# Performance work log

Measured on AMD Instinct MI355X. Metric: run time of the kernel, lower is better.

Reference implementation:

```python
import jax, jax.numpy as jnp
import numpy as np

B = 1 << 20
EMB = 8
N_BREEDS, N_TEMPS = 15, 9
HIDDENS = [128, 64, 32]
IN_DIM = (EMB * 2 + 9) * 2  # 50
EPS = 1e-5


def _encode_pet(breed, size, energy, temp, age, social, weight, breed_emb, temp_emb):
    # breed/temp: [B] int -> embedding gather [B,8]; size/energy -> one-hot [B,3]
    be = breed_emb[breed]
    te = temp_emb[temp]
    size_oh = jax.nn.one_hot(size, 3, dtype=be.dtype)
    energy_oh = jax.nn.one_hot(energy, 3, dtype=be.dtype)
    nums = jnp.stack([age / 15.0, social, weight / 100.0], axis=-1)  # [B,3]
    return jnp.concatenate([be, size_oh, energy_oh, te, nums], axis=-1)  # [B,25]


def _mlp(x, Ws, bs, gammas, betas, Wout, bout):
    for W, b, g, bt in zip(Ws, bs, gammas, betas):
        x = x @ W + b
        mu = jnp.mean(x, axis=0)
        var = jnp.mean(jnp.square(x - mu), axis=0)  # biased var (torch BN training)
        x = (x - mu) * jax.lax.rsqrt(var + EPS) * g + bt
        x = jax.nn.relu(x)
    x = x @ Wout + bout
    return jax.nn.sigmoid(x).squeeze(-1)  # [B]


def setup_inputs() -> dict:
    key = jax.random.key(0)
    ks = jax.random.split(key, 32)
    inp = {
        "pet1_breed": jax.random.randint(ks[0], (B,), 0, N_BREEDS, dtype=jnp.int32),
        "pet1_size": jax.random.randint(ks[1], (B,), 0, 3, dtype=jnp.int32),
        "pet1_energy": jax.random.randint(ks[2], (B,), 0, 3, dtype=jnp.int32),
        "pet1_temp": jax.random.randint(ks[3], (B,), 0, N_TEMPS, dtype=jnp.int32),
        "pet1_age": jax.random.uniform(ks[4], (B,)) * 15.0,
        "pet1_social": jax.random.uniform(ks[5], (B,)),
        "pet1_weight": jax.random.uniform(ks[6], (B,)) * 100.0,
        "pet2_breed": jax.random.randint(ks[7], (B,), 0, N_BREEDS, dtype=jnp.int32),
        "pet2_size": jax.random.randint(ks[8], (B,), 0, 3, dtype=jnp.int32),
        "pet2_energy": jax.random.randint(ks[9], (B,), 0, 3, dtype=jnp.int32),
        "pet2_temp": jax.random.randint(ks[10], (B,), 0, N_TEMPS, dtype=jnp.int32),
        "pet2_age": jax.random.uniform(ks[11], (B,)) * 15.0,
        "pet2_social": jax.random.uniform(ks[12], (B,)),
        "pet2_weight": jax.random.uniform(ks[13], (B,)) * 100.0,
        "breed_emb": jax.random.normal(ks[14], (N_BREEDS, EMB), dtype=jnp.float32),
        "temp_emb": jax.random.normal(ks[15], (N_TEMPS, EMB), dtype=jnp.float32),
    }
    prev = IN_DIM
    ki = 16
    for i, h in enumerate(HIDDENS, start=1):
        s = 1.0 / np.sqrt(prev)
        inp[f"W{i}"] = jax.random.uniform(ks[ki], (prev, h), minval=-s, maxval=s); ki += 1
        inp[f"b{i}"] = jax.random.uniform(ks[ki], (h,), minval=-s, maxval=s); ki += 1
        inp[f"gamma{i}"] = jnp.ones((h,), jnp.float32)
        inp[f"beta{i}"] = jnp.zeros((h,), jnp.float32)
        prev = h
    s = 1.0 / np.sqrt(prev)
    inp["W4"] = jax.random.uniform(ks[ki], (prev, 1), minval=-s, maxval=s); ki += 1
    inp["b4"] = jax.random.uniform(ks[ki], (1,), minval=-s, maxval=s)
    return inp


def reference(pet1_breed, pet1_size, pet1_energy, pet1_temp, pet1_age, pet1_social, pet1_weight,
              pet2_breed, pet2_size, pet2_energy, pet2_temp, pet2_age, pet2_social, pet2_weight,
              breed_emb, temp_emb,
              W1, b1, gamma1, beta1, W2, b2, gamma2, beta2, W3, b3, gamma3, beta3, W4, b4):
    f1 = _encode_pet(pet1_breed, pet1_size, pet1_energy, pet1_temp,
                     pet1_age, pet1_social, pet1_weight, breed_emb, temp_emb)
    f2 = _encode_pet(pet2_breed, pet2_size, pet2_energy, pet2_temp,
                     pet2_age, pet2_social, pet2_weight, breed_emb, temp_emb)
    x = jnp.concatenate([f1, f2], axis=-1)  # [B,50]
    return _mlp(x, [W1, W2, W3], [b1, b2, b3], [gamma1, gamma2, gamma3],
                [beta1, beta2, beta3], W4, b4)
```

## Files before the change

kernel.cpp:

```cpp
#include <hip/hip_runtime.h>
#include <hip/hip_bf16.h>

#define BATCH (1u<<20)
static constexpr float EPSBN = 1e-5f;
static constexpr float INV_B = 1.0f / (float)BATCH;

typedef unsigned int   uint;
typedef unsigned short ushort;

#define TSTR 132
#define NTABROWS 66
#define OFF_W2F    55296ULL
#define OFF_W3F    71680ULL
#define OFF_STATS  75776ULL
#define OFF_PARAMS 90112ULL
#define OFF_X2     98304ULL
#define OFF_X3D    (98304ULL + 134217728ULL)
#define T1_NEED    (98304ULL + 134217728ULL)
#define T2_NEED    (98304ULL + 134217728ULL + 67108864ULL)

struct Ptrs {
  const int *br1,*sz1,*en1,*tp1; const float *ag1,*so1,*wt1;
  const int *br2,*sz2,*en2,*tp2; const float *ag2,*so2,*wt2;
  const float *bemb,*temb;
  const float *W1,*b1,*g1,*be1;
  const float *W2,*b2,*g2,*be2;
  const float *W3,*b3,*g3,*be3;
  const float *W4,*b4;
  float* ws; float* out;
};

typedef __attribute__((ext_vector_type(8))) short bf16x8;
typedef __attribute__((ext_vector_type(4))) float f32x4;

__device__ __forceinline__ float4 ld4(const float* p) {
  return *reinterpret_cast<const float4*>(p);
}
__device__ __forceinline__ float4 f4add(float4 a, float4 b) {
  return make_float4(a.x+b.x, a.y+b.y, a.z+b.z, a.w+b.w);
}
__device__ __forceinline__ float4 f4fma(float4 a, float4 w, float s) {
  return make_float4(fmaf(w.x,s,a.x), fmaf(w.y,s,a.y), fmaf(w.z,s,a.z), fmaf(w.w,s,a.w));
}
__device__ __forceinline__ void add4(float4& a, const float4 b) {
  a.x += b.x; a.y += b.y; a.z += b.z; a.w += b.w;
}
__device__ __forceinline__ void fma4s(float4& a, const float4 b, float s) {
  a.x = fmaf(b.x, s, a.x); a.y = fmaf(b.y, s, a.y);
  a.z = fmaf(b.z, s, a.z); a.w = fmaf(b.w, s, a.w);
}

__device__ __forceinline__ ushort bfb(float f) {
  union { __hip_bfloat16 h; ushort u; } cv; cv.h = __float2bfloat16(f); return cv.u;
}
__device__ __forceinline__ uint pk2(float a, float b) {
  return ((uint)bfb(b) << 16) | (uint)bfb(a);
}
__device__ __forceinline__ bf16x8 ldfrag(const void* p) {
  union { uint4 u; bf16x8 v; } cv; cv.u = *reinterpret_cast<const uint4*>(p); return cv.v;
}
__device__ __forceinline__ bf16x8 mkfrag(uint a, uint b, uint c, uint d) {
  union { uint4 u; bf16x8 v; } cv; cv.u = make_uint4(a,b,c,d); return cv.v;
}
__device__ __forceinline__ float bflo(uint w) { return __uint_as_float(w << 16); }
__device__ __forceinline__ float bfhi(uint w) { return __uint_as_float(w & 0xffff0000u); }

struct SIdx { int r[8]; float v[6]; };
__device__ __forceinline__ SIdx load_idx(const Ptrs& P, unsigned s) {
  SIdx o;
  o.r[0] = P.br1[s];      o.r[1] = 15 + P.tp1[s];
  o.r[2] = 24 + P.br2[s]; o.r[3] = 39 + P.tp2[s];
  o.r[4] = 48 + P.sz1[s]; o.r[5] = 51 + P.en1[s];
  o.r[6] = 54 + P.sz2[s]; o.r[7] = 57 + P.en2[s];
  o.v[0] = P.ag1[s]*(1.0f/15.0f); o.v[1] = P.so1[s]; o.v[2] = P.wt1[s]*0.01f;
  o.v[3] = P.ag2[s]*(1.0f/15.0f); o.v[4] = P.so2[s]; o.v[5] = P.wt2[s]*0.01f;
  return o;
}

__device__ __forceinline__ float4 gather4(const float* Tl, const float* contT,
                                          const int rb[8], const float v[6], int c) {
  float4 A = f4add(f4add(ld4(Tl+rb[0]+c), ld4(Tl+rb[1]+c)),
                   f4add(ld4(Tl+rb[2]+c), ld4(Tl+rb[3]+c)));
  float4 B = f4add(f4add(ld4(Tl+rb[4]+c), ld4(Tl+rb[5]+c)),
                   f4add(ld4(Tl+rb[6]+c), ld4(Tl+rb[7]+c)));
  A = f4fma(A, ld4(contT + 60*TSTR + c), v[0]);
  A = f4fma(A, ld4(contT + 61*TSTR + c), v[1]);
  A = f4fma(A, ld4(contT + 62*TSTR + c), v[2]);
  B = f4fma(B, ld4(contT + 63*TSTR + c), v[3]);
  B = f4fma(B, ld4(contT + 64*TSTR + c), v[4]);
  B = f4fma(B, ld4(contT + 65*TSTR + c), v[5]);
  return f4add(A, B);
}

__device__ __forceinline__ void load_rb(const Ptrs& P, unsigned s, int rb[8], float v[6]) {
  SIdx o = load_idx(P, s);
  #pragma unroll
  for (int i = 0; i < 8; ++i) rb[i] = o.r[i]*TSTR;
  #pragma unroll
  for (int i = 0; i < 6; ++i) v[i] = o.v[i];
}

__device__ __forceinline__ void stage_tab(const float* wsT, const float* params,
                                          float* Tl, bool bn1) {
  for (int i = threadIdx.x; i < NTABROWS*TSTR; i += blockDim.x) Tl[i] = wsT[i];
  if (bn1) {
    for (int i = threadIdx.x; i < 128; i += blockDim.x) {
      Tl[66*TSTR + i] = params[i];
      Tl[67*TSTR + i] = params[128 + i];
    }
  }
  __syncthreads();
}

__device__ __forceinline__ void x2_from_lds(const float* Tl, const int rb[8], const float v[6],
                                            const float* W2, const float* b2, float4 acc[16]) {
  #pragma unroll
  for (int j4 = 0; j4 < 16; ++j4) acc[j4] = ld4(b2 + j4*4);
  #pragma unroll 1
  for (int c4 = 0; c4 < 32; ++c4) {
    const int c = c4 * 4;
    float4 x = gather4(Tl, Tl, rb, v, c);
    const float4 sc = *reinterpret_cast<const float4*>(Tl + 66*TSTR + c);
    const float4 sh = *reinterpret_cast<const float4*>(Tl + 67*TSTR + c);
    float hv[4];
    hv[0] = fmaxf(fmaf(x.x, sc.x, sh.x), 0.0f);
    hv[1] = fmaxf(fmaf(x.y, sc.y, sh.y), 0.0f);
    hv[2] = fmaxf(fmaf(x.z, sc.z, sh.z), 0.0f);
    hv[3] = fmaxf(fmaf(x.w, sc.w, sh.w), 0.0f);
    #pragma unroll
    for (int r = 0; r < 4; ++r) {
// ... 47 lines not shown
  const bool hi = (lane & 32) != 0;
  #pragma unroll
  for (int j4 = 0; j4 < 8; ++j4) {
#define DO1(comp, idx) { \
    float lo = acc[j4].comp, hc = acc[j4+8].comp; \
    if (SQ) { lo *= lo; hc *= hc; } \
    float mine = hi ? lo : hc; \
    float keep = hi ? hc : lo; \
    st[4*j4+idx] = keep + __shfl_xor(mine, 32, 64); }
    DO1(x,0) DO1(y,1) DO1(z,2) DO1(w,3)
#undef DO1
  }
  return bfly_tail32(st, lane);
}

template<bool SQ>
__device__ __forceinline__ float bfly32_from(const float4 acc3[8], int lane) {
  float st[32];
  const bool hi = (lane & 32) != 0;
  #pragma unroll
  for (int j4 = 0; j4 < 8; ++j4) {
#define DO1(comp, idx) { \
    float vv = acc3[j4].comp; \
    if (SQ) vv *= vv; \
    float mine = hi ? vv : 0.0f; \
    float keep = hi ? 0.0f : vv; \
    st[4*j4+idx] = keep + __shfl_xor(mine, 32, 64); }
    DO1(x,0) DO1(y,1) DO1(z,2) DO1(w,3)
#undef DO1
  }
  return bfly_tail32(st, lane);
}


__global__ __launch_bounds__(256) void k_prep(Ptrs P) {
  const int t = threadIdx.x;
  float* T = P.ws;
  {
    float* st = (float*)((char*)P.ws + OFF_STATS);
    for (int i = t; i < 224*16; i += 256) st[i] = 0.0f;
  }
  if (t < 128) {
    const int c = t;
    for (int b = 0; b < 15; ++b) {
      float a1 = P.b1[c], a2 = 0.0f;
      #pragma unroll
      for (int e = 0; e < 8; ++e) {
        a1 = fmaf(P.bemb[b*8+e], P.W1[e*128 + c], a1);
        a2 = fmaf(P.bemb[b*8+e], P.W1[(25+e)*128 + c], a2);
      }
      T[b*TSTR + c] = a1; T[(24+b)*TSTR + c] = a2;
    }
    for (int tt = 0; tt < 9; ++tt) {
      float a1 = 0.0f, a2 = 0.0f;
      #pragma unroll
      for (int e = 0; e < 8; ++e) {
        a1 = fmaf(P.temb[tt*8+e], P.W1[(14+e)*128 + c], a1);
        a2 = fmaf(P.temb[tt*8+e], P.W1[(39+e)*128 + c], a2);
      }
      T[(15+tt)*TSTR + c] = a1; T[(39+tt)*TSTR + c] = a2;
    }
    #pragma unroll
    for (int i = 0; i < 3; ++i) {
      T[(48+i)*TSTR + c] = P.W1[(8+i)*128 + c];
      T[(51+i)*TSTR + c] = P.W1[(11+i)*128 + c];
      T[(54+i)*TSTR + c] = P.W1[(33+i)*128 + c];
      T[(57+i)*TSTR + c] = P.W1[(36+i)*128 + c];
    }
    const int cr[6] = {22,23,24,47,48,49};
    #pragma unroll
    for (int m = 0; m < 6; ++m) T[(60+m)*TSTR + c] = P.W1[cr[m]*128 + c];
  }
  __syncthreads();
  __hip_bfloat16* w2f = (__hip_bfloat16*)((char*)P.ws + OFF_W2F);
  for (int slot = t; slot < 1024; slot += 256) {
    const int fid = slot >> 6, l = slot & 63;
    const int mt = fid >> 2, kk = fid & 3, q = l >> 4, m = l & 15;
    #pragma unroll
    for (int e = 0; e < 8; ++e)
      w2f[slot*8 + e] = __float2bfloat16(P.W2[(kk*32 + 8*q + e)*64 + 16*mt + m]);
  }
  __hip_bfloat16* w3f = (__hip_bfloat16*)((char*)P.ws + OFF_W3F);
  for (int slot = t; slot < 256; slot += 256) {
    const int fid = slot >> 6, l = slot & 63;
    const int mt = fid >> 1, kk = fid & 1, q = l >> 4, m = l & 15;
    #pragma unroll
    for (int e = 0; e < 8; ++e)
      w3f[slot*8 + e] = __float2bfloat16(P.W3[(kk*32 + 8*q + e)*32 + 16*mt + m]);
  }
}

__global__ __launch_bounds__(512) void k_stats1(Ptrs P) {
  __shared__ __align__(16) float Tl[60*TSTR];
  __shared__ float sred[256];
  for (int i = threadIdx.x; i < 60*TSTR; i += 512) Tl[i] = P.ws[i];
  if (threadIdx.x < 256) sred[threadIdx.x] = 0.f;
  __syncthreads();
  const int lane = threadIdx.x & 63;
  const int q = lane >> 4, m16 = lane & 15;
  const float* contT = P.ws;
  const unsigned gw = (blockIdx.x*512 + threadIdx.x) >> 6;
  const unsigned nw = (gridDim.x*512) >> 6;
  const int kk = gw & 3;
  const int c = kk*32 + 8*q;
  const unsigned NT = BATCH >> 4;
  unsigned it = gw >> 2;
  const unsigned ts = nw >> 2;
  float4 sa = make_float4(0,0,0,0), sb = sa, qa = sa, qb = sa;
  bool active = it < NT;
  SIdx cur;
  if (active) cur = load_idx(P, it*16 + m16);
  while (active) {
    const unsigned itn = it + ts;
    const bool more = itn < NT;
    SIdx nxt;
    if (more) nxt = load_idx(P, itn*16 + m16);
    int rb[8];
    #pragma unroll
    for (int i = 0; i < 8; ++i) rb[i] = cur.r[i]*TSTR;
    const float4 xa = gather4(Tl, contT, rb, cur.v, c);
    const float4 xb = gather4(Tl, contT, rb, cur.v, c + 4);
    add4(sa, xa); add4(sb, xb);
    qa.x = fmaf(xa.x, xa.x, qa.x); qa.y = fmaf(xa.y, xa.y, qa.y);
    qa.z = fmaf(xa.z, xa.z, qa.z); qa.w = fmaf(xa.w, xa.w, qa.w);
    qb.x = fmaf(xb.x, xb.x, qb.x); qb.y = fmaf(xb.y, xb.y, qb.y);
    qb.z = fmaf(xb.z, xb.z, qb.z); qb.w = fmaf(xb.w, xb.w, qb.w);
    if (!more) break;
    cur = nxt; it = itn;
  }
  #pragma unroll
  for (int d = 1; d <= 8; d <<= 1) {
    sa.x += __shfl_xor(sa.x, d, 64); sa.y += __shfl_xor(sa.y, d, 64);
    sa.z += __shfl_xor(sa.z, d, 64); sa.w += __shfl_xor(sa.w, d, 64);
    sb.x += __shfl_xor(sb.x, d, 64); sb.y += __shfl_xor(sb.y, d, 64);
    sb.z += __shfl_xor(sb.z, d, 64); sb.w += __shfl_xor(sb.w, d, 64);
    qa.x += __shfl_xor(qa.x, d, 64); qa.y += __shfl_xor(qa.y, d, 64);
    qa.z += __shfl_xor(qa.z, d, 64); qa.w += __shfl_xor(qa.w, d, 64);
    qb.x += __shfl_xor(qb.x, d, 64); qb.y += __shfl_xor(qb.y, d, 64);
    qb.z += __shfl_xor(qb.z, d, 64); qb.w += __shfl_xor(qb.w, d, 64);
  }
  if (m16 == 0) {
    atomicAdd(&sred[c+0], sa.x); atomicAdd(&sred[c+1], sa.y);
    atomicAdd(&sred[c+2], sa.z); atomicAdd(&sred[c+3], sa.w);
    atomicAdd(&sred[c+4], sb.x); atomicAdd(&sred[c+5], sb.y);
    atomicAdd(&sred[c+6], sb.z); atomicAdd(&sred[c+7], sb.w);
    atomicAdd(&sred[128+c+0], qa.x); atomicAdd(&sred[128+c+1], qa.y);
    atomicAdd(&sred[128+c+2], qa.z); atomicAdd(&sred[128+c+3], qa.w);
    atomicAdd(&sred[128+c+4], qb.x); atomicAdd(&sred[128+c+5], qb.y);
    atomicAdd(&sred[128+c+6], qb.z); atomicAdd(&sred[128+c+7], qb.w);
  }
  __syncthreads();
  if (threadIdx.x < 128) {
    float* stat = (float*)((char*)P.ws + OFF_STATS) + (size_t)threadIdx.x*16;
    atomicAdd(stat,     sred[threadIdx.x]);
    atomicAdd(stat + 8, sred[128+threadIdx.x]);
  }
}

__global__ void k_finalize(Ptrs P, int nch, int entry0, int pofs,
                           const float* g, const float* be) {
  const int c = threadIdx.x;
  if (c >= nch) return;
  const float* stat = (const float*)((const char*)P.ws + OFF_STATS) + (size_t)(entry0 + c)*16;
  const float mean = stat[0] * INV_B;
  const float var  = stat[8] * INV_B - mean*mean;
  const float inv  = 1.0f / sqrtf(var + EPSBN);
  const float scale = g[c] * inv;
  float* params = (float*)((char*)P.ws + OFF_PARAMS);
  params[pofs + c]       = scale;
  params[pofs + nch + c] = be[c] - mean * scale;
}

__global__ __launch_bounds__(512) void k_l2m(Ptrs P) {
  __shared__ __align__(16) float Tl[60*TSTR];
  __shared__ __align__(16) float bn[256];
  for (int i = threadIdx.x; i < 60*TSTR; i += 512) Tl[i] = P.ws[i];
  if (threadIdx.x < 128) {
    const float* stat = (const float*)((const char*)P.ws + OFF_STATS) + (size_t)threadIdx.x*16;
    const float mean = stat[0] * INV_B;
    const float var  = stat[8] * INV_B - mean*mean;
    const float scale = P.g1[threadIdx.x] / sqrtf(var + EPSBN);
    bn[threadIdx.x]       = scale;
    bn[128 + threadIdx.x] = P.be1[threadIdx.x] - mean * scale;
  }
  __syncthreads();
  const float* contT = P.ws;
  const int lane = threadIdx.x & 63;
  const int q = lane >> 4, m16 = lane & 15;
  const char* w2fB = (const char*)P.ws + OFF_W2F;
  char* x2B = (char*)P.ws + OFF_X2;
  const unsigned nw = (gridDim.x*512) >> 6;
  const unsigned NT = BATCH >> 4;
  unsigned it = (blockIdx.x*512 + threadIdx.x) >> 6;
  if (it >= NT) return;
  SIdx cur = load_idx(P, it*16 + m16);
  while (true) {
    const unsigned itn = it + nw;
    const bool more = itn < NT;
    SIdx nxt;
    if (more) nxt = load_idx(P, itn*16 + m16);
    const unsigned s = it*16 + m16;
    int rb[8];
    #pragma unroll
    for (int i = 0; i < 8; ++i) rb[i] = cur.r[i]*TSTR;
    f32x4 D[4];
    #pragma unroll
    for (int mt = 0; mt < 4; ++mt) {
      const float4 b = ld4(P.b2 + 16*mt + 4*q);
      D[mt][0] = b.x; D[mt][1] = b.y; D[mt][2] = b.z; D[mt][3] = b.w;
    }
    #pragma unroll
    for (int kk = 0; kk < 4; ++kk) {
      const int c = kk*32 + 8*q;
      const float4 xa = gather4(Tl, contT, rb, cur.v, c);
      const float4 xb = gather4(Tl, contT, rb, cur.v, c + 4);
      const float4 sca = ld4(bn + c), sha = ld4(bn + 128 + c);
      const float4 scb = ld4(bn + c + 4), shb = ld4(bn + 128 + c + 4);
      const float h0 = fmaxf(fmaf(xa.x, sca.x, sha.x), 0.f);
      const float h1 = fmaxf(fmaf(xa.y, sca.y, sha.y), 0.f);
      const float h2 = fmaxf(fmaf(xa.z, sca.z, sha.z), 0.f);
      const float h3 = fmaxf(fmaf(xa.w, sca.w, sha.w), 0.f);
      const float h4 = fmaxf(fmaf(xb.x, scb.x, shb.x), 0.f);
      const float h5 = fmaxf(fmaf(xb.y, scb.y, shb.y), 0.f);
      const float h6 = fmaxf(fmaf(xb.z, scb.z, shb.z), 0.f);
      const float h7 = fmaxf(fmaf(xb.w, scb.w, shb.w), 0.f);
      const bf16x8 bf = mkfrag(pk2(h0,h1), pk2(h2,h3), pk2(h4,h5), pk2(h6,h7));
      #pragma unroll
      for (int mt = 0; mt < 4; ++mt) {
        const bf16x8 af = ldfrag(w2fB + (size_t)((mt*4+kk)*64 + lane)*16);
        D[mt] = __builtin_amdgcn_mfma_f32_16x16x32_bf16(af, bf, D[mt], 0, 0, 0);
      }
    }
    #pragma unroll
    for (int mt = 0; mt < 4; ++mt) {
      const uint lo = pk2(D[mt][0], D[mt][1]);
      const uint hi = pk2(D[mt][2], D[mt][3]);
      *reinterpret_cast<uint2*>(x2B + (size_t)s*128 + (16*mt + 4*q)*2) = make_uint2(lo, hi);
    }
    if (!more) break;
    cur = nxt; it = itn;
  }
}

__global__ __launch_bounds__(256) void k_stats2(Ptrs P) {
  const uint* x2u = (const uint*)((const char*)P.ws + OFF_X2);
  const int pid = threadIdx.x & 31;
  const int lane = threadIdx.x & 63;
  const int w = threadIdx.x >> 6;
  float slo = 0.f, shi = 0.f, qlo = 0.f, qhi = 0.f;
  const unsigned r0 = blockIdx.x*8 + (threadIdx.x >> 5);
  const unsigned rs = gridDim.x*8;
  #pragma unroll 4
  for (unsigned r = r0; r < BATCH; r += rs) {
    const uint u = x2u[(size_t)r*32 + pid];
    const float lo = bflo(u), hi = bfhi(u);
    slo += lo; shi += hi;
    qlo = fmaf(lo, lo, qlo); qhi = fmaf(hi, hi, qhi);
  }
  slo += __shfl_xor(slo, 32, 64); shi += __shfl_xor(shi, 32, 64);
  qlo += __shfl_xor(qlo, 32, 64); qhi += __shfl_xor(qhi, 32, 64);
  __shared__ float red[512];
  if (lane < 32) {
    red[w*64 + 2*pid]       = slo; red[w*64 + 2*pid + 1]       = shi;
    red[256 + w*64 + 2*pid] = qlo; red[256 + w*64 + 2*pid + 1] = qhi;
  }
  __syncthreads();
  if (threadIdx.x < 64) {
    const int c = threadIdx.x;
    const float s  = red[c] + red[64+c] + red[128+c] + red[192+c];
    const float qq = red[256+c] + red[320+c] + red[384+c] + red[448+c];
// ... 251 lines not shown
      z = fmaf(fmaxf(fmaf(a.y, sc.y, sh.y), 0.0f), P.W4[k4*4+1], z);
      z = fmaf(fmaxf(fmaf(a.z, sc.z, sh.z), 0.0f), P.W4[k4*4+2], z);
      z = fmaf(fmaxf(fmaf(a.w, sc.w, sh.w), 0.0f), P.W4[k4*4+3], z);
    }
    P.out[s] = 1.0f / (1.0f + __expf(-z));
  }
}


extern "C" void kernel_launch(void* const* d_in, const int* in_sizes, int n_in,
                              void* d_out, int out_size, void* d_ws, size_t ws_size,
                              hipStream_t stream) {
  Ptrs P;
  P.br1 = (const int*)d_in[0];  P.sz1 = (const int*)d_in[1];
  P.en1 = (const int*)d_in[2];  P.tp1 = (const int*)d_in[3];
  P.ag1 = (const float*)d_in[4]; P.so1 = (const float*)d_in[5]; P.wt1 = (const float*)d_in[6];
  P.br2 = (const int*)d_in[7];  P.sz2 = (const int*)d_in[8];
  P.en2 = (const int*)d_in[9];  P.tp2 = (const int*)d_in[10];
  P.ag2 = (const float*)d_in[11]; P.so2 = (const float*)d_in[12]; P.wt2 = (const float*)d_in[13];
  P.bemb = (const float*)d_in[14]; P.temb = (const float*)d_in[15];
  P.W1 = (const float*)d_in[16]; P.b1 = (const float*)d_in[17];
  P.g1 = (const float*)d_in[18]; P.be1 = (const float*)d_in[19];
  P.W2 = (const float*)d_in[20]; P.b2 = (const float*)d_in[21];
  P.g2 = (const float*)d_in[22]; P.be2 = (const float*)d_in[23];
  P.W3 = (const float*)d_in[24]; P.b3 = (const float*)d_in[25];
  P.g3 = (const float*)d_in[26]; P.be3 = (const float*)d_in[27];
  P.W4 = (const float*)d_in[28]; P.b4 = (const float*)d_in[29];
  P.ws = (float*)d_ws; P.out = (float*)d_out;

  const bool t1 = ws_size >= T1_NEED;
  const int dense = (ws_size >= T2_NEED) ? 1 : 0;

  hipLaunchKernelGGL(k_prep, dim3(1), dim3(256), 0, stream, P);
  hipLaunchKernelGGL(k_stats1, dim3(1024), dim3(512), 0, stream, P);
  if (t1) {
    hipLaunchKernelGGL(k_l2m, dim3(1024), dim3(512), 0, stream, P);
    hipLaunchKernelGGL(k_stats2, dim3(1024), dim3(256), 0, stream, P);
    hipLaunchKernelGGL(k_l3m, dim3(2048), dim3(256), 0, stream, P, dense);
    hipLaunchKernelGGL(k_stats3, dim3(1024), dim3(256), 0, stream, P, dense);
    hipLaunchKernelGGL(k_l4n, dim3(2048), dim3(256), 0, stream, P, dense);
  } else {
    hipLaunchKernelGGL(k_finalize, dim3(1), dim3(128), 0, stream, P, 128, 0, 0, P.g1, P.be1);
    hipLaunchKernelGGL(k_l2r, dim3(1024), dim3(256), 0, stream, P);
    hipLaunchKernelGGL(k_finalize, dim3(1), dim3(64), 0, stream, P, 64, 128, 256, P.g2, P.be2);
    hipLaunchKernelGGL(k_l3_rec, dim3(1024), dim3(256), 0, stream, P);
    hipLaunchKernelGGL(k_finalize, dim3(1), dim3(32), 0, stream, P, 32, 192, 384, P.g3, P.be3);
    hipLaunchKernelGGL(k_l4_rec, dim3(2048), dim3(256), 0, stream, P);
  }
}
```

Measured before the change: 606.6 us.

## Compute layer-1 via MFMA with BN-folded split-bf16 weights instead of LDS gathers

```diff
diff --git a/kernel.cpp b/kernel.cpp
--- a/kernel.cpp
+++ b/kernel.cpp
@@ -10,14 +10,15 @@
 
 #define TSTR 132
 #define NTABROWS 66
-#define OFF_W2F    55296ULL
-#define OFF_W3F    71680ULL
-#define OFF_STATS  75776ULL
-#define OFF_PARAMS 90112ULL
-#define OFF_X2     98304ULL
-#define OFF_X3D    (98304ULL + 134217728ULL)
-#define T1_NEED    (98304ULL + 134217728ULL)
-#define T2_NEED    (98304ULL + 134217728ULL + 67108864ULL)
+#define OFF_W1F    36864ULL
+#define OFF_W2F    86016ULL
+#define OFF_W3F    102400ULL
+#define OFF_STATS  106496ULL
+#define OFF_PARAMS 120832ULL
+#define OFF_X2     131072ULL
+#define OFF_X3D    (131072ULL + 134217728ULL)
+#define T1_NEED    (131072ULL + 134217728ULL)
+#define T2_NEED    (131072ULL + 134217728ULL + 67108864ULL)
 
 struct Ptrs {
   const int *br1,*sz1,*en1,*tp1; const float *ag1,*so1,*wt1;
@@ -56,6 +57,9 @@
 __device__ __forceinline__ uint pk2(float a, float b) {
   return ((uint)bfb(b) << 16) | (uint)bfb(a);
 }
+__device__ __forceinline__ uint pku(ushort a, ushort b) {
+  return ((uint)b << 16) | (uint)a;
+}
 __device__ __forceinline__ bf16x8 ldfrag(const void* p) {
   union { uint4 u; bf16x8 v; } cv; cv.u = *reinterpret_cast<const uint4*>(p); return cv.v;
 }
@@ -64,14 +68,13 @@
 }
 __device__ __forceinline__ float bflo(uint w) { return __uint_as_float(w << 16); }
 __device__ __forceinline__ float bfhi(uint w) { return __uint_as_float(w & 0xffff0000u); }
-
-struct SIdx { int r[8]; float v[6]; };
-__device__ __forceinline__ SIdx load_idx(const Ptrs& P, unsigned s) {
+__device__ __forceinline__ float bf2f(ushort u) { return __uint_as_float(((uint)u) << 16); }
+
+struct SIdx { int c[8]; float v[6]; };
+__device__ __forceinline__ SIdx load_raw(const Ptrs& P, unsigned s) {
   SIdx o;
-  o.r[0] = P.br1[s];      o.r[1] = 15 + P.tp1[s];
-  o.r[2] = 24 + P.br2[s]; o.r[3] = 39 + P.tp2[s];
-  o.r[4] = 48 + P.sz1[s]; o.r[5] = 51 + P.en1[s];
-  o.r[6] = 54 + P.sz2[s]; o.r[7] = 57 + P.en2[s];
+  o.c[0] = P.br1[s]; o.c[1] = P.tp1[s]; o.c[2] = P.br2[s]; o.c[3] = P.tp2[s];
+  o.c[4] = P.sz1[s]; o.c[5] = P.en1[s]; o.c[6] = P.sz2[s]; o.c[7] = P.en2[s];
   o.v[0] = P.ag1[s]*(1.0f/15.0f); o.v[1] = P.so1[s]; o.v[2] = P.wt1[s]*0.01f;
   o.v[3] = P.ag2[s]*(1.0f/15.0f); o.v[4] = P.so2[s]; o.v[5] = P.wt2[s]*0.01f;
   return o;
@@ -93,9 +96,11 @@
 }
 
 __device__ __forceinline__ void load_rb(const Ptrs& P, unsigned s, int rb[8], float v[6]) {
-  SIdx o = load_idx(P, s);
-  #pragma unroll
-  for (int i = 0; i < 8; ++i) rb[i] = o.r[i]*TSTR;
+  SIdx o = load_raw(P, s);
+  rb[0] = o.c[0]*TSTR;        rb[1] = (15+o.c[1])*TSTR;
+  rb[2] = (24+o.c[2])*TSTR;   rb[3] = (39+o.c[3])*TSTR;
+  rb[4] = (48+o.c[4])*TSTR;   rb[5] = (51+o.c[5])*TSTR;
+  rb[6] = (54+o.c[6])*TSTR;   rb[7] = (57+o.c[7])*TSTR;
   #pragma unroll
   for (int i = 0; i < 6; ++i) v[i] = o.v[i];
 }
@@ -285,25 +290,26 @@
   const unsigned ts = nw >> 2;
   float4 sa = make_float4(0,0,0,0), sb = sa, qa = sa, qb = sa;
   bool active = it < NT;
-  SIdx cur;
-  if (active) cur = load_idx(P, it*16 + m16);
+  int rb[8]; float v[6];
+  if (active) load_rb(P, it*16 + m16, rb, v);
   while (active) {
     const unsigned itn = it + ts;
     const bool more = itn < NT;
-    SIdx nxt;
-    if (more) nxt = load_idx(P, itn*16 + m16);
-    int rb[8];
-    #pragma unroll
-    for (int i = 0; i < 8; ++i) rb[i] = cur.r[i]*TSTR;
-    const float4 xa = gather4(Tl, contT, rb, cur.v, c);
-    const float4 xb = gather4(Tl, contT, rb, cur.v, c + 4);
+    int rbn[8]; float vn[6];
+    if (more) load_rb(P, itn*16 + m16, rbn, vn);
+    const float4 xa = gather4(Tl, contT, rb, v, c);
+    const float4 xb = gather4(Tl, contT, rb, v, c + 4);
     add4(sa, xa); add4(sb, xb);
     qa.x = fmaf(xa.x, xa.x, qa.x); qa.y = fmaf(xa.y, xa.y, qa.y);
     qa.z = fmaf(xa.z, xa.z, qa.z); qa.w = fmaf(xa.w, xa.w, qa.w);
     qb.x = fmaf(xb.x, xb.x, qb.x); qb.y = fmaf(xb.y, xb.y, qb.y);
     qb.z = fmaf(xb.z, xb.z, qb.z); qb.w = fmaf(xb.w, xb.w, qb.w);
     if (!more) break;
-    cur = nxt; it = itn;
+    #pragma unroll
+    for (int i = 0; i < 8; ++i) rb[i] = rbn[i];
+    #pragma unroll
+    for (int i = 0; i < 6; ++i) v[i] = vn[i];
+    it = itn;
   }
   #pragma unroll
   for (int d = 1; d <= 8; d <<= 1) {
@@ -332,6 +338,41 @@
     atomicAdd(stat,     sred[threadIdx.x]);
     atomicAdd(stat + 8, sred[128+threadIdx.x]);
   }
+}
+
+__global__ __launch_bounds__(256) void k_frag(Ptrs P) {
+  const int slot = blockIdx.x*256 + threadIdx.x;
+  if (slot >= 3072) return;
+  const int fid = slot >> 6, l = slot & 63;
+  const int hl = fid & 1, mk = fid >> 1;
+  const int kk = mk % 3, mt = mk / 3;
+  const int q = l >> 4, m = l & 15, ch = 16*mt + m;
+  const float* stat = (const float*)((const char*)P.ws + OFF_STATS) + (size_t)ch*16;
+  const float mean = stat[0] * INV_B;
+  const float var  = stat[8] * INV_B - mean*mean;
+  const float sc = P.g1[ch] / sqrtf(var + EPSBN);
+  const float sh = P.be1[ch] - mean * sc;
+  ushort out[8];
+  #pragma unroll
+  for (int e = 0; e < 8; ++e) {
+    const int t = 8*kk + e;
+    int row = -1; bool shrow = false;
+    if (t < 4)       { const int b = 4*t + q; if (t == 3 && q == 3) shrow = true; else if (b <= 14) row = b; }
+    else if (t < 7)  { if (t == 6 && q >= 1) row = 60 + (q-1); else { const int vv = 4*(t-4)+q; if (vv <= 8) row = 15 + vv; } }
+    else if (t == 7) { if (q <= 2) row = 48 + q; }
+    else if (t < 12) { const int b = 4*(t-8)+q; if (b <= 14) row = 24 + b; }
+    else if (t < 15) { if (t == 14 && q >= 1) row = 63 + (q-1); else { const int vv = 4*(t-12)+q; if (vv <= 8) row = 39 + vv; } }
+    else if (t == 15){ if (q <= 2) row = 51 + q; }
+    else if (t == 16){ if (q <= 2) row = 54 + q; }
+    else if (t == 17){ if (q <= 2) row = 57 + q; }
+    float val = shrow ? sh : ((row >= 0) ? P.ws[row*TSTR + ch] * sc : 0.0f);
+    const ushort hibits = bfb(val);
+    if (hl == 0) out[e] = hibits;
+    else out[e] = bfb(val - bf2f(hibits));
+  }
+  uint4* dst = (uint4*)((char*)P.ws + OFF_W1F);
+  dst[slot] = make_uint4(pku(out[0],out[1]), pku(out[2],out[3]),
+                         pku(out[4],out[5]), pku(out[6],out[7]));
 }
 
 __global__ void k_finalize(Ptrs P, int nch, int entry0, int pofs,
@@ -349,70 +390,103 @@
 }
 
 __global__ __launch_bounds__(512) void k_l2m(Ptrs P) {
-  __shared__ __align__(16) float Tl[60*TSTR];
-  __shared__ __align__(16) float bn[256];
-  for (int i = threadIdx.x; i < 60*TSTR; i += 512) Tl[i] = P.ws[i];
-  if (threadIdx.x < 128) {
-    const float* stat = (const float*)((const char*)P.ws + OFF_STATS) + (size_t)threadIdx.x*16;
-    const float mean = stat[0] * INV_B;
-    const float var  = stat[8] * INV_B - mean*mean;
-    const float scale = P.g1[threadIdx.x] / sqrtf(var + EPSBN);
-    bn[threadIdx.x]       = scale;
-    bn[128 + threadIdx.x] = P.be1[threadIdx.x] - mean * scale;
-  }
-  __syncthreads();
-  const float* contT = P.ws;
+  __shared__ __align__(16) char FR[65536];
+  {
+    const uint4* s1 = (const uint4*)((const char*)P.ws + OFF_W1F);
+    const uint4* s2 = (const uint4*)((const char*)P.ws + OFF_W2F);
+    uint4* d = (uint4*)FR;
+    for (int i = threadIdx.x; i < 4096; i += 512)
+      d[i] = (i < 3072) ? s1[i] : s2[i - 3072];
+  }
+  __syncthreads();
+  const char* w1fB = FR;
+  const char* w2fB = FR + 49152;
   const int lane = threadIdx.x & 63;
   const int q = lane >> 4, m16 = lane & 15;
-  const char* w2fB = (const char*)P.ws + OFF_W2F;
   char* x2B = (char*)P.ws + OFF_X2;
   const unsigned nw = (gridDim.x*512) >> 6;
   const unsigned NT = BATCH >> 4;
   unsigned it = (blockIdx.x*512 + threadIdx.x) >> 6;
   if (it >= NT) return;
-  SIdx cur = load_idx(P, it*16 + m16);
+  SIdx cur = load_raw(P, it*16 + m16);
   while (true) {
     const unsigned itn = it + nw;
     const bool more = itn < NT;
     SIdx nxt;
-    if (more) nxt = load_idx(P, itn*16 + m16);
+    if (more) nxt = load_raw(P, itn*16 + m16);
     const unsigned s = it*16 + m16;
-    int rb[8];
-    #pragma unroll
-    for (int i = 0; i < 8; ++i) rb[i] = cur.r[i]*TSTR;
-    f32x4 D[4];
-    #pragma unroll
-    for (int mt = 0; mt < 4; ++mt) {
-      const float4 b = ld4(P.b2 + 16*mt + 4*q);
-      D[mt][0] = b.x; D[mt][1] = b.y; D[mt][2] = b.z; D[mt][3] = b.w;
-    }
-    #pragma unroll
-    for (int kk = 0; kk < 4; ++kk) {
-      const int c = kk*32 + 8*q;
-      const float4 xa = gather4(Tl, contT, rb, cur.v, c);
-      const float4 xb = gather4(Tl, contT, rb, cur.v, c + 4);
-      const float4 sca = ld4(bn + c), sha = ld4(bn + 128 + c);
-      const float4 scb = ld4(bn + c + 4), shb = ld4(bn + 128 + c + 4);
-      const float h0 = fmaxf(fmaf(xa.x, sca.x, sha.x), 0.f);
-      const float h1 = fmaxf(fmaf(xa.y, sca.y, sha.y), 0.f);
-      const float h2 = fmaxf(fmaf(xa.z, sca.z, sha.z), 0.f);
-      const float h3 = fmaxf(fmaf(xa.w, sca.w, sha.w), 0.f);
-      const float h4 = fmaxf(fmaf(xb.x, scb.x, shb.x), 0.f);
-      const float h5 = fmaxf(fmaf(xb.y, scb.y, shb.y), 0.f);
-      const float h6 = fmaxf(fmaf(xb.z, scb.z, shb.z), 0.f);
-      const float h7 = fmaxf(fmaf(xb.w, scb.w, shb.w), 0.f);
-      const bf16x8 bf = mkfrag(pk2(h0,h1), pk2(h2,h3), pk2(h4,h5), pk2(h6,h7));
+    const ushort ONE = 0x3F80;
+    const ushort vb0 = bfb(cur.v[0]), vb1 = bfb(cur.v[1]), vb2 = bfb(cur.v[2]);
+    const ushort vb3 = bfb(cur.v[3]), vb4 = bfb(cur.v[4]), vb5 = bfb(cur.v[5]);
+#define INDE(cv, tgt) ((ushort)(((cv) == (tgt)) ? ONE : 0))
+    const ushort e0 = INDE(cur.c[0], q),     e1 = INDE(cur.c[0], 4+q);
+    const ushort e2 = INDE(cur.c[0], 8+q);
+    const ushort e3 = (q == 3) ? ONE : INDE(cur.c[0], 12+q);
+    const ushort e4 = INDE(cur.c[1], q),     e5 = INDE(cur.c[1], 4+q);
+    const ushort e6 = (q == 0) ? INDE(cur.c[1], 8)
+                               : ((q == 1) ? vb0 : (q == 2) ? vb1 : vb2);
+    const ushort e7 = INDE(cur.c[4], q);
+    const ushort f0 = INDE(cur.c[2], q),     f1 = INDE(cur.c[2], 4+q);
+    const ushort f2 = INDE(cur.c[2], 8+q),   f3 = INDE(cur.c[2], 12+q);
+    const ushort f4 = INDE(cur.c[3], q),     f5 = INDE(cur.c[3], 4+q);
+    const ushort f6 = (q == 0) ? INDE(cur.c[3], 8)
+                               : ((q == 1) ? vb3 : (q == 2) ? vb4 : vb5);
+    const ushort f7 = INDE(cur.c[5], q);
+    const ushort g0 = INDE(cur.c[6], q),     g1 = INDE(cur.c[7], q);
+#undef INDE
+    const bf16x8 B0 = mkfrag(pku(e0,e1), pku(e2,e3), pku(e4,e5), pku(e6,e7));
+    const bf16x8 B1 = mkfrag(pku(f0,f1), pku(f2,f3), pku(f4,f5), pku(f6,f7));
+    const bf16x8 B2 = mkfrag(pku(g0,g1), 0u, 0u, 0u);
+    f32x4 D1[8];
+    #pragma unroll
+    for (int mt = 0; mt < 8; ++mt) D1[mt] = (f32x4){0.f,0.f,0.f,0.f};
+    #pragma unroll
+    for (int kk = 0; kk < 3; ++kk) {
+      const bf16x8 bf = (kk == 0) ? B0 : (kk == 1) ? B1 : B2;
       #pragma unroll
-      for (int mt = 0; mt < 4; ++mt) {
-        const bf16x8 af = ldfrag(w2fB + (size_t)((mt*4+kk)*64 + lane)*16);
-        D[mt] = __builtin_amdgcn_mfma_f32_16x16x32_bf16(af, bf, D[mt], 0, 0, 0);
+      for (int mt = 0; mt < 8; ++mt) {
+        const bf16x8 ah = ldfrag(w1fB + (size_t)(((mt*3+kk)*2+0)*64 + lane)*16);
+        D1[mt] = __builtin_amdgcn_mfma_f32_16x16x32_bf16(ah, bf, D1[mt], 0, 0, 0);
+        const bf16x8 al = ldfrag(w1fB + (size_t)(((mt*3+kk)*2+1)*64 + lane)*16);
+        D1[mt] = __builtin_amdgcn_mfma_f32_16x16x32_bf16(al, bf, D1[mt], 0, 0, 0);
       }
     }
-    #pragma unroll
-    for (int mt = 0; mt < 4; ++mt) {
-      const uint lo = pk2(D[mt][0], D[mt][1]);
-      const uint hi = pk2(D[mt][2], D[mt][3]);
-      *reinterpret_cast<uint2*>(x2B + (size_t)s*128 + (16*mt + 4*q)*2) = make_uint2(lo, hi);
+    uint pkh[8][2];
+    #pragma unroll
+    for (int mt = 0; mt < 8; ++mt) {
+      const float h0 = fmaxf(D1[mt][0], 0.f), h1 = fmaxf(D1[mt][1], 0.f);
+      const float h2 = fmaxf(D1[mt][2], 0.f), h3 = fmaxf(D1[mt][3], 0.f);
+      pkh[mt][0] = pk2(h0, h1);
+      pkh[mt][1] = pk2(h2, h3);
+    }
+    f32x4 D2[4];
+    #pragma unroll
+    for (int mt2 = 0; mt2 < 4; ++mt2) {
+      const float4 b = ld4(P.b2 + 16*mt2 + 4*q);
+      D2[mt2][0] = b.x; D2[mt2][1] = b.y; D2[mt2][2] = b.z; D2[mt2][3] = b.w;
+    }
+    #pragma unroll
+    for (int kk2 = 0; kk2 < 4; ++kk2) {
+      uint fw[4];
+      #pragma unroll
+      for (int w2 = 0; w2 < 4; ++w2) {
+        const int src = ((2*(q & 1) + (w2 >> 1)) << 4) | m16;
+        const uint ua = (uint)__shfl((int)pkh[2*kk2][w2 & 1], src, 64);
+        const uint ub = (uint)__shfl((int)pkh[2*kk2+1][w2 & 1], src, 64);
+        fw[w2] = (q & 2) ? ub : ua;
+      }
+      const bf16x8 bf = mkfrag(fw[0], fw[1], fw[2], fw[3]);
+      #pragma unroll
+      for (int mt2 = 0; mt2 < 4; ++mt2) {
+        const bf16x8 af = ldfrag(w2fB + (size_t)((mt2*4+kk2)*64 + lane)*16);
+        D2[mt2] = __builtin_amdgcn_mfma_f32_16x16x32_bf16(af, bf, D2[mt2], 0, 0, 0);
+      }
+    }
+    #pragma unroll
+    for (int mt2 = 0; mt2 < 4; ++mt2) {
+      const uint lo = pk2(D2[mt2][0], D2[mt2][1]);
+      const uint hi = pk2(D2[mt2][2], D2[mt2][3]);
+      *reinterpret_cast<uint2*>(x2B + (size_t)s*128 + (16*mt2 + 4*q)*2) = make_uint2(lo, hi);
     }
     if (!more) break;
     cur = nxt; it = itn;
@@ -732,6 +806,7 @@
   hipLaunchKernelGGL(k_prep, dim3(1), dim3(256), 0, stream, P);
   hipLaunchKernelGGL(k_stats1, dim3(1024), dim3(512), 0, stream, P);
   if (t1) {
+    hipLaunchKernelGGL(k_frag, dim3(12), dim3(256), 0, stream, P);
     hipLaunchKernelGGL(k_l2m, dim3(1024), dim3(512), 0, stream, P);
     hipLaunchKernelGGL(k_stats2, dim3(1024), dim3(256), 0, stream, P);
     hipLaunchKernelGGL(k_l3m, dim3(2048), dim3(256), 0, stream, P, dense);
```

After: 717.8 us. 18.3% more time.

## Compute layer-1 BN stats from a 67x67 feature Gram matrix instead of gathering

Applied to the files above, without the earlier changes.

```diff
diff --git a/kernel.cpp b/kernel.cpp
--- a/kernel.cpp
+++ b/kernel.cpp
@@ -14,10 +14,11 @@
 #define OFF_W3F    71680ULL
 #define OFF_STATS  75776ULL
 #define OFF_PARAMS 90112ULL
-#define OFF_X2     98304ULL
-#define OFF_X3D    (98304ULL + 134217728ULL)
-#define T1_NEED    (98304ULL + 134217728ULL)
-#define T2_NEED    (98304ULL + 134217728ULL + 67108864ULL)
+#define OFF_GRAM   94208ULL
+#define OFF_X2     131072ULL
+#define OFF_X3D    (131072ULL + 134217728ULL)
+#define T1_NEED    (131072ULL + 134217728ULL)
+#define T2_NEED    (131072ULL + 134217728ULL + 67108864ULL)
 
 struct Ptrs {
   const int *br1,*sz1,*en1,*tp1; const float *ag1,*so1,*wt1;
@@ -216,6 +217,8 @@
   {
     float* st = (float*)((char*)P.ws + OFF_STATS);
     for (int i = t; i < 224*16; i += 256) st[i] = 0.0f;
+    float* G = (float*)((char*)P.ws + OFF_GRAM);
+    for (int i = t; i < 67*67; i += 256) G[i] = 0.0f;
   }
   if (t < 128) {
     const int c = t;
@@ -265,6 +268,74 @@
     for (int e = 0; e < 8; ++e)
       w3f[slot*8 + e] = __float2bfloat16(P.W3[(kk*32 + 8*q + e)*32 + 16*mt + m]);
   }
+}
+
+__global__ __launch_bounds__(256) void k_gram(Ptrs P) {
+  __shared__ float Gl[67*67];
+  for (int i = threadIdx.x; i < 67*67; i += 256) Gl[i] = 0.f;
+  __syncthreads();
+  float fx[28];
+  #pragma unroll
+  for (int i = 0; i < 28; ++i) fx[i] = 0.f;
+  const unsigned gid = blockIdx.x*256 + threadIdx.x;
+  const unsigned nth = gridDim.x*256;
+  for (unsigned s = gid; s < BATCH; s += nth) {
+    const SIdx o = load_idx(P, s);
+    #pragma unroll
+    for (int a = 0; a < 8; ++a) {
+      const int ra = o.r[a]*67;
+      #pragma unroll
+      for (int b = a; b < 8; ++b) atomicAdd(&Gl[ra + o.r[b]], 1.0f);
+      #pragma unroll
+      for (int m = 0; m < 6; ++m) atomicAdd(&Gl[ra + 60 + m], o.v[m]);
+      atomicAdd(&Gl[ra + 66], 1.0f);
+    }
+    int p = 0;
+    #pragma unroll
+    for (int m = 0; m < 6; ++m)
+      #pragma unroll
+      for (int n = m; n < 6; ++n) { fx[p] = fmaf(o.v[m], o.v[n], fx[p]); ++p; }
+    #pragma unroll
+    for (int m = 0; m < 6; ++m) fx[21+m] += o.v[m];
+    fx[27] += 1.0f;
+  }
+  {
+    int p = 0;
+    #pragma unroll
+    for (int m = 0; m < 6; ++m)
+      #pragma unroll
+      for (int n = m; n < 6; ++n) { atomicAdd(&Gl[(60+m)*67 + 60+n], fx[p]); ++p; }
+    #pragma unroll
+    for (int m = 0; m < 6; ++m) atomicAdd(&Gl[(60+m)*67 + 66], fx[21+m]);
+    atomicAdd(&Gl[66*67 + 66], fx[27]);
+  }
+  __syncthreads();
+  float* G = (float*)((char*)P.ws + OFF_GRAM);
+  for (int i = threadIdx.x; i < 67*67; i += 256) {
+    const float g = Gl[i];
+    if (g != 0.f) atomicAdd(&G[i], g);
+  }
+}
+
+__global__ __launch_bounds__(128) void k_bn1fin(Ptrs P) {
+  __shared__ float Gl[67*67];
+  const float* G = (const float*)((const char*)P.ws + OFF_GRAM);
+  for (int i = threadIdx.x; i < 67*67; i += 128) Gl[i] = G[i];
+  __syncthreads();
+  const int c = threadIdx.x;
+  float sum = 0.f, sq = 0.f;
+  #pragma unroll 1
+  for (int i = 0; i < 66; ++i) {
+    const float ti = P.ws[i*TSTR + c];
+    sum = fmaf(Gl[i*67 + 66], ti, sum);
+    float acc = Gl[i*67 + i] * ti;
+    #pragma unroll 1
+    for (int j = i + 1; j < 66; ++j)
+      acc = fmaf(2.0f*Gl[i*67 + j], P.ws[j*TSTR + c], acc);
+    sq = fmaf(acc, ti, sq);
+  }
+  float* stat = (float*)((char*)P.ws + OFF_STATS) + (size_t)c*16;
+  stat[0] = sum; stat[8] = sq;
 }
 
 __global__ __launch_bounds__(512) void k_stats1(Ptrs P) {
@@ -285,25 +356,26 @@
   const unsigned ts = nw >> 2;
   float4 sa = make_float4(0,0,0,0), sb = sa, qa = sa, qb = sa;
   bool active = it < NT;
-  SIdx cur;
-  if (active) cur = load_idx(P, it*16 + m16);
+  int rb[8]; float v[6];
+  if (active) load_rb(P, it*16 + m16, rb, v);
   while (active) {
     const unsigned itn = it + ts;
     const bool more = itn < NT;
-    SIdx nxt;
-    if (more) nxt = load_idx(P, itn*16 + m16);
-    int rb[8];
-    #pragma unroll
-    for (int i = 0; i < 8; ++i) rb[i] = cur.r[i]*TSTR;
-    const float4 xa = gather4(Tl, contT, rb, cur.v, c);
-    const float4 xb = gather4(Tl, contT, rb, cur.v, c + 4);
+    int rbn[8]; float vn[6];
+    if (more) load_rb(P, itn*16 + m16, rbn, vn);
+    const float4 xa = gather4(Tl, contT, rb, v, c);
+    const float4 xb = gather4(Tl, contT, rb, v, c + 4);
     add4(sa, xa); add4(sb, xb);
     qa.x = fmaf(xa.x, xa.x, qa.x); qa.y = fmaf(xa.y, xa.y, qa.y);
     qa.z = fmaf(xa.z, xa.z, qa.z); qa.w = fmaf(xa.w, xa.w, qa.w);
     qb.x = fmaf(xb.x, xb.x, qb.x); qb.y = fmaf(xb.y, xb.y, qb.y);
     qb.z = fmaf(xb.z, xb.z, qb.z); qb.w = fmaf(xb.w, xb.w, qb.w);
     if (!more) break;
-    cur = nxt; it = itn;
+    #pragma unroll
+    for (int i = 0; i < 8; ++i) rb[i] = rbn[i];
+    #pragma unroll
+    for (int i = 0; i < 6; ++i) v[i] = vn[i];
+    it = itn;
   }
   #pragma unroll
   for (int d = 1; d <= 8; d <<= 1) {
@@ -730,14 +802,16 @@
   const int dense = (ws_size >= T2_NEED) ? 1 : 0;
 
   hipLaunchKernelGGL(k_prep, dim3(1), dim3(256), 0, stream, P);
-  hipLaunchKernelGGL(k_stats1, dim3(1024), dim3(512), 0, stream, P);
   if (t1) {
+    hipLaunchKernelGGL(k_gram, dim3(512), dim3(256), 0, stream, P);
+    hipLaunchKernelGGL(k_bn1fin, dim3(1), dim3(128), 0, stream, P);
     hipLaunchKernelGGL(k_l2m, dim3(1024), dim3(512), 0, stream, P);
     hipLaunchKernelGGL(k_stats2, dim3(1024), dim3(256), 0, stream, P);
     hipLaunchKernelGGL(k_l3m, dim3(2048), dim3(256), 0, stream, P, dense);
     hipLaunchKernelGGL(k_stats3, dim3(1024), dim3(256), 0, stream, P, dense);
     hipLaunchKernelGGL(k_l4n, dim3(2048), dim3(256), 0, stream, P, dense);
   } else {
+    hipLaunchKernelGGL(k_stats1, dim3(1024), dim3(512), 0, stream, P);
     hipLaunchKernelGGL(k_finalize, dim3(1), dim3(128), 0, stream, P, 128, 0, 0, P.g1, P.be1);
     hipLaunchKernelGGL(k_l2r, dim3(1024), dim3(256), 0, stream, P);
     hipLaunchKernelGGL(k_finalize, dim3(1), dim3(64), 0, stream, P, 64, 128, 256, P.g2, P.be2);
```

Result: slower. 1.146 ms (+89.0%).

## Compute layer-1 batch-norm statistics with bf16 MFMA on one-hot inputs

Applied to the files above, without the earlier changes.

```diff
diff --git a/kernel.cpp b/kernel.cpp
--- a/kernel.cpp
+++ b/kernel.cpp
@@ -14,10 +14,11 @@
 #define OFF_W3F    71680ULL
 #define OFF_STATS  75776ULL
 #define OFF_PARAMS 90112ULL
-#define OFF_X2     98304ULL
-#define OFF_X3D    (98304ULL + 134217728ULL)
-#define T1_NEED    (98304ULL + 134217728ULL)
-#define T2_NEED    (98304ULL + 134217728ULL + 67108864ULL)
+#define OFF_W1S    94208ULL
+#define OFF_X2     147456ULL
+#define OFF_X3D    (147456ULL + 134217728ULL)
+#define T1_NEED    (147456ULL + 134217728ULL)
+#define T2_NEED    (147456ULL + 134217728ULL + 67108864ULL)
 
 struct Ptrs {
   const int *br1,*sz1,*en1,*tp1; const float *ag1,*so1,*wt1;
@@ -56,6 +57,9 @@
 __device__ __forceinline__ uint pk2(float a, float b) {
   return ((uint)bfb(b) << 16) | (uint)bfb(a);
 }
+__device__ __forceinline__ uint pku(ushort a, ushort b) {
+  return ((uint)b << 16) | (uint)a;
+}
 __device__ __forceinline__ bf16x8 ldfrag(const void* p) {
   union { uint4 u; bf16x8 v; } cv; cv.u = *reinterpret_cast<const uint4*>(p); return cv.v;
 }
@@ -64,6 +68,7 @@
 }
 __device__ __forceinline__ float bflo(uint w) { return __uint_as_float(w << 16); }
 __device__ __forceinline__ float bfhi(uint w) { return __uint_as_float(w & 0xffff0000u); }
+__device__ __forceinline__ float bf2f(ushort u) { return __uint_as_float(((uint)u) << 16); }
 
 struct SIdx { int r[8]; float v[6]; };
 __device__ __forceinline__ SIdx load_idx(const Ptrs& P, unsigned s) {
@@ -209,6 +214,18 @@
   return bfly_tail32(st, lane);
 }
 
+__device__ __forceinline__ int frag_row(int t, int q) {
+  if (t < 4)       { if (t == 3 && q == 3) return -1; const int b = 4*t + q; return (b <= 14) ? b : -1; }
+  else if (t < 7)  { if (t == 6 && q >= 1) return 60 + (q-1); const int vv = 4*(t-4)+q; return (vv <= 8) ? 15 + vv : -1; }
+  else if (t == 7) { return (q <= 2) ? 48 + q : -1; }
+  else if (t < 12) { const int b = 4*(t-8)+q; return (b <= 14) ? 24 + b : -1; }
+  else if (t < 15) { if (t == 14 && q >= 1) return 63 + (q-1); const int vv = 4*(t-12)+q; return (vv <= 8) ? 39 + vv : -1; }
+  else if (t == 15){ return (q <= 2) ? 51 + q : -1; }
+  else if (t == 16){ return (q <= 2) ? 54 + q : -1; }
+  else if (t == 17){ return (q <= 2) ? 57 + q : -1; }
+  return -1;
+}
+
 
 __global__ __launch_bounds__(256) void k_prep(Ptrs P) {
   const int t = threadIdx.x;
@@ -264,6 +281,116 @@
     #pragma unroll
     for (int e = 0; e < 8; ++e)
       w3f[slot*8 + e] = __float2bfloat16(P.W3[(kk*32 + 8*q + e)*32 + 16*mt + m]);
+  }
+  uint4* w1s = (uint4*)((char*)P.ws + OFF_W1S);
+  for (int slot = t; slot < 3072; slot += 256) {
+    const int fid = slot >> 6, l = slot & 63;
+    const int hl = fid & 1, mk = fid >> 1;
+    const int kk = mk % 3, mt = mk / 3;
+    const int q = l >> 4, m = l & 15, ch = 16*mt + m;
+    ushort out[8];
+    #pragma unroll
+    for (int e = 0; e < 8; ++e) {
+      const int row = frag_row(8*kk + e, q);
+      const float val = (row >= 0) ? T[row*TSTR + ch] : 0.0f;
+      const ushort hib = bfb(val);
+      out[e] = (hl == 0) ? hib : bfb(val - bf2f(hib));
+    }
+    w1s[slot] = make_uint4(pku(out[0],out[1]), pku(out[2],out[3]),
+                           pku(out[4],out[5]), pku(out[6],out[7]));
+  }
+}
+
+__global__ __launch_bounds__(512) void k_stats1m(Ptrs P) {
+  __shared__ __align__(16) char Wl[49152];
+  __shared__ float sred[256];
+  {
+    const uint4* src = (const uint4*)((const char*)P.ws + OFF_W1S);
+    uint4* dst = (uint4*)Wl;
+    for (int i = threadIdx.x; i < 3072; i += 512) dst[i] = src[i];
+  }
+  if (threadIdx.x < 256) sred[threadIdx.x] = 0.f;
+  __syncthreads();
+  const int lane = threadIdx.x & 63;
+  const int q = lane >> 4, m16 = lane & 15;
+  f32x4 sums[8], sqs[8];
+  #pragma unroll
+  for (int mt = 0; mt < 8; ++mt) { sums[mt] = (f32x4){0,0,0,0}; sqs[mt] = (f32x4){0,0,0,0}; }
+  const unsigned nw = (gridDim.x*512) >> 6;
+  const unsigned NT = BATCH >> 4;
+  const ushort ONE = 0x3F80;
+  for (unsigned it = (blockIdx.x*512 + threadIdx.x) >> 6; it < NT; it += nw) {
+    const unsigned s = it*16 + m16;
+    const int c0 = P.br1[s], c1 = P.tp1[s], c2 = P.br2[s], c3 = P.tp2[s];
+    const int c4i = P.sz1[s], c5 = P.en1[s], c6 = P.sz2[s], c7 = P.en2[s];
+    const ushort vb0 = bfb(P.ag1[s]*(1.0f/15.0f)), vb1 = bfb(P.so1[s]);
+    const ushort vb2 = bfb(P.wt1[s]*0.01f);
+    const ushort vb3 = bfb(P.ag2[s]*(1.0f/15.0f)), vb4 = bfb(P.so2[s]);
+    const ushort vb5 = bfb(P.wt2[s]*0.01f);
+#define INDE(cv, tgt) ((ushort)(((cv) == (tgt)) ? ONE : 0))
+    const ushort e0 = INDE(c0, q),     e1 = INDE(c0, 4+q);
+    const ushort e2 = INDE(c0, 8+q);
+    const ushort e3 = (q == 3) ? ONE : INDE(c0, 12+q);
+    const ushort e4 = INDE(c1, q),     e5 = INDE(c1, 4+q);
+    const ushort e6 = (q == 0) ? INDE(c1, 8)
+                               : ((q == 1) ? vb0 : (q == 2) ? vb1 : vb2);
+    const ushort e7 = INDE(c4i, q);
+    const ushort f0 = INDE(c2, q),     f1 = INDE(c2, 4+q);
+    const ushort f2 = INDE(c2, 8+q),   f3 = INDE(c2, 12+q);
+    const ushort f4 = INDE(c3, q),     f5 = INDE(c3, 4+q);
+    const ushort f6 = (q == 0) ? INDE(c3, 8)
+                               : ((q == 1) ? vb3 : (q == 2) ? vb4 : vb5);
+    const ushort f7 = INDE(c5, q);
+    const ushort g0 = INDE(c6, q),     g1 = INDE(c7, q);
+#undef INDE
+    const bf16x8 B0 = mkfrag(pku(e0,e1), pku(e2,e3), pku(e4,e5), pku(e6,e7));
+    const bf16x8 B1 = mkfrag(pku(f0,f1), pku(f2,f3), pku(f4,f5), pku(f6,f7));
+    const bf16x8 B2 = mkfrag(pku(g0,g1), 0u, 0u, 0u);
+    #pragma unroll
+    for (int mt = 0; mt < 8; ++mt) {
+      f32x4 D = (f32x4){0.f,0.f,0.f,0.f};
+      #pragma unroll
+      for (int kk = 0; kk < 3; ++kk) {
+        const bf16x8 bf = (kk == 0) ? B0 : (kk == 1) ? B1 : B2;
+        const bf16x8 ah = ldfrag(Wl + (size_t)(((mt*3+kk)*2+0)*64 + lane)*16);
+        D = __builtin_amdgcn_mfma_f32_16x16x32_bf16(ah, bf, D, 0, 0, 0);
+        const bf16x8 al = ldfrag(Wl + (size_t)(((mt*3+kk)*2+1)*64 + lane)*16);
+        D = __builtin_amdgcn_mfma_f32_16x16x32_bf16(al, bf, D, 0, 0, 0);
+      }
+      #pragma unroll
+      for (int r = 0; r < 4; ++r) {
+        sums[mt][r] += D[r];
+        sqs[mt][r]   = fmaf(D[r], D[r], sqs[mt][r]);
+      }
+    }
+  }
+  #pragma unroll
+  for (int d = 1; d <= 8; d <<= 1) {
+    #pragma unroll
+    for (int mt = 0; mt < 8; ++mt) {
+      #pragma unroll
+      for (int r = 0; r < 4; ++r) {
+        sums[mt][r] += __shfl_xor(sums[mt][r], d, 64);
+        sqs[mt][r]  += __shfl_xor(sqs[mt][r],  d, 64);
+      }
+    }
+  }
+  if (m16 == 0) {
+    #pragma unroll
+    for (int mt = 0; mt < 8; ++mt) {
+      #pragma unroll
+      for (int r = 0; r < 4; ++r) {
+        const int ch = 16*mt + 4*q + r;
+        atomicAdd(&sred[ch], sums[mt][r]);
+        atomicAdd(&sred[128+ch], sqs[mt][r]);
+      }
+    }
+  }
+  __syncthreads();
+  if (threadIdx.x < 128) {
+    float* stat = (float*)((char*)P.ws + OFF_STATS) + (size_t)threadIdx.x*16;
+    atomicAdd(stat,     sred[threadIdx.x]);
+    atomicAdd(stat + 8, sred[128+threadIdx.x]);
   }
 }
 
@@ -285,25 +412,26 @@
   const unsigned ts = nw >> 2;
   float4 sa = make_float4(0,0,0,0), sb = sa, qa = sa, qb = sa;
   bool active = it < NT;
-  SIdx cur;
-  if (active) cur = load_idx(P, it*16 + m16);
+  int rb[8]; float v[6];
+  if (active) load_rb(P, it*16 + m16, rb, v);
   while (active) {
     const unsigned itn = it + ts;
     const bool more = itn < NT;
-    SIdx nxt;
-    if (more) nxt = load_idx(P, itn*16 + m16);
-    int rb[8];
-    #pragma unroll
-    for (int i = 0; i < 8; ++i) rb[i] = cur.r[i]*TSTR;
-    const float4 xa = gather4(Tl, contT, rb, cur.v, c);
-    const float4 xb = gather4(Tl, contT, rb, cur.v, c + 4);
+    int rbn[8]; float vn[6];
+    if (more) load_rb(P, itn*16 + m16, rbn, vn);
+    const float4 xa = gather4(Tl, contT, rb, v, c);
+    const float4 xb = gather4(Tl, contT, rb, v, c + 4);
     add4(sa, xa); add4(sb, xb);
     qa.x = fmaf(xa.x, xa.x, qa.x); qa.y = fmaf(xa.y, xa.y, qa.y);
     qa.z = fmaf(xa.z, xa.z, qa.z); qa.w = fmaf(xa.w, xa.w, qa.w);
     qb.x = fmaf(xb.x, xb.x, qb.x); qb.y = fmaf(xb.y, xb.y, qb.y);
     qb.z = fmaf(xb.z, xb.z, qb.z); qb.w = fmaf(xb.w, xb.w, qb.w);
     if (!more) break;
-    cur = nxt; it = itn;
+    #pragma unroll
+    for (int i = 0; i < 8; ++i) rb[i] = rbn[i];
+    #pragma unroll
+    for (int i = 0; i < 6; ++i) v[i] = vn[i];
+    it = itn;
   }
   #pragma unroll
   for (int d = 1; d <= 8; d <<= 1) {
@@ -730,14 +858,15 @@
   const int dense = (ws_size >= T2_NEED) ? 1 : 0;
 
   hipLaunchKernelGGL(k_prep, dim3(1), dim3(256), 0, stream, P);
-  hipLaunchKernelGGL(k_stats1, dim3(1024), dim3(512), 0, stream, P);
   if (t1) {
+    hipLaunchKernelGGL(k_stats1m, dim3(1024), dim3(512), 0, stream, P);
     hipLaunchKernelGGL(k_l2m, dim3(1024), dim3(512), 0, stream, P);
     hipLaunchKernelGGL(k_stats2, dim3(1024), dim3(256), 0, stream, P);
     hipLaunchKernelGGL(k_l3m, dim3(2048), dim3(256), 0, stream, P, dense);
     hipLaunchKernelGGL(k_stats3, dim3(1024), dim3(256), 0, stream, P, dense);
     hipLaunchKernelGGL(k_l4n, dim3(2048), dim3(256), 0, stream, P, dense);
   } else {
+    hipLaunchKernelGGL(k_stats1, dim3(1024), dim3(512), 0, stream, P);
     hipLaunchKernelGGL(k_finalize, dim3(1), dim3(128), 0, stream, P, 128, 0, 0, P.g1, P.be1);
     hipLaunchKernelGGL(k_l2r, dim3(1024), dim3(256), 0, stream, P);
     hipLaunchKernelGGL(k_finalize, dim3(1), dim3(64), 0, stream, P, 64, 128, 256, P.g2, P.be2);
```

New measurement: 664.5 us. 1.1x slower.
